# Kernel tuning notes

Hardware: AMD Instinct MI355X
Metric: run time of the kernel (lower is better)

## Reference

```python
import jax, jax.numpy as jnp
import numpy as np
from jax import lax

B, P, DIM, HEADS, K = 2, 4096, 256, 8, 32
DH = DIM // HEADS
SCALE = DH ** -0.5


def setup_inputs() -> dict:
    key = jax.random.key(0)
    ks = jax.random.split(key, 12)
    s = 0.02
    return {
        "xyz": jax.random.uniform(ks[0], (B, P, 3), dtype=jnp.float32),
        "feats": jax.random.normal(ks[1], (B, P, DIM), dtype=jnp.float32),
        "Wq": jax.random.normal(ks[2], (DIM, DIM), dtype=jnp.float32) * s,
        "Wk": jax.random.normal(ks[3], (DIM, DIM), dtype=jnp.float32) * s,
        "Wv": jax.random.normal(ks[4], (DIM, DIM), dtype=jnp.float32) * s,
        "Wp": jax.random.normal(ks[5], (DIM, DIM), dtype=jnp.float32) * s,
        "bp": jnp.zeros((DIM,), jnp.float32),
        "W1": jax.random.normal(ks[6], (DIM, 3), dtype=jnp.float32) * s,
        "b1": jnp.zeros((DIM,), jnp.float32),
        "W2": jax.random.normal(ks[7], (DIM, DIM), dtype=jnp.float32) * s,
        "b2": jnp.zeros((DIM,), jnp.float32),
    }


def _gather(points, idx):
    # points: (B,N,C), idx: (B,M,K) -> (B,M,K,C)
    return jax.vmap(lambda p, i: p[i])(points, idx)


def reference(xyz, feats, Wq, Wk, Wv, Wp, bp, W1, b1, W2, b2):
    b, p, d = feats.shape
    # kNN via squared euclidean distance (same ordering as cdist)
    d2 = jnp.sum((xyz[:, :, None, :] - xyz[:, None, :, :]) ** 2, axis=-1)  # (B,P,P)
    _, idx = lax.top_k(-d2, K)  # (B,P,K) smallest distances

    neigh_xyz = _gather(xyz, idx)                      # (B,P,K,3)
    relpos = neigh_xyz - xyz[:, :, None, :]            # (B,P,K,3)

    q = (feats @ Wq.T).reshape(b, p, HEADS, DH)        # (B,P,H,Dh)
    k_full = feats @ Wk.T                              # (B,P,D)
    v_full = feats @ Wv.T
    k_nei = _gather(k_full, idx).reshape(b, p, K, HEADS, DH)
    v_nei = _gather(v_full, idx).reshape(b, p, K, HEADS, DH)

    # pos MLP: Linear(3,dim) -> ReLU -> Linear(dim,dim)
    h = jax.nn.relu(relpos @ W1.T + b1)
    pos_bias = (h @ W2.T + b2).reshape(b, p, K, HEADS, DH)

    attn = jnp.einsum('bphd,bpkhd->bpkh', q, k_nei + pos_bias) * SCALE
    attn = jax.nn.softmax(attn, axis=2)                # over K neighbors
    out = jnp.einsum('bpkh,bpkhd->bphd', attn, v_nei + pos_bias).reshape(b, p, d)
    return out @ Wp.T + bp
```

## Files before the change

### kernel.cpp

```cpp
#include <hip/hip_runtime.h>
#include <cstddef>

#define PB 4096
static constexpr float SCALE_F = 0.17677669529663687f;

typedef __attribute__((ext_vector_type(8))) short bf16x8;
typedef __attribute__((ext_vector_type(4))) float f32x4;

static __device__ __forceinline__ unsigned short f2bf(float x) {
  unsigned u = __builtin_bit_cast(unsigned, x);
  u += 0x7fffu + ((u >> 16) & 1u);
  return (unsigned short)(u >> 16);
}
static __device__ __forceinline__ float bf2f(unsigned short h) {
  return __builtin_bit_cast(float, (unsigned)h << 16);
}

__global__ __launch_bounds__(64) void knn_kernel(const float* __restrict__ xyz,
                                                 int* __restrict__ idx_out) {
  const int g = blockIdx.x;
  const int b = g >> 12;
  const int p = g & (PB - 1);
  const int lane = threadIdx.x;
  const float* base = xyz + (size_t)b * PB * 3;
  const float qx = base[p * 3 + 0];
  const float qy = base[p * 3 + 1];
  const float qz = base[p * 3 + 2];
  float list_d = 3.4e38f;
  int list_i = -1;
  for (int c = 0; c < PB / 64; ++c) {
    const int j = (c << 6) + lane;
    const float dx = __fsub_rn(qx, base[j * 3 + 0]);
    const float dy = __fsub_rn(qy, base[j * 3 + 1]);
    const float dz = __fsub_rn(qz, base[j * 3 + 2]);
    const float d2 = __fadd_rn(__fadd_rn(__fmul_rn(dx, dx), __fmul_rn(dy, dy)),
                               __fmul_rn(dz, dz));
    float worst = __shfl(list_d, 31);
    unsigned long long mask = __ballot(d2 < worst);
    while (mask) {
      const int l = __ffsll(mask) - 1;
      mask &= mask - 1;
      const float v = __shfl(d2, l);
      worst = __shfl(list_d, 31);
      if (v < worst) {
        const unsigned long long gt = __ballot((lane < 32) && (list_d > v));
        const int pos = __ffsll(gt) - 1;
        const float pd = __shfl_up(list_d, 1);
        const int pi = __shfl_up(list_i, 1);
        if (lane < 32 && lane >= pos) {
          const bool at = (lane == pos);
          list_d = at ? v : pd;
          list_i = at ? ((c << 6) + l) : pi;
        }
      }
    }
  }
  if (lane < 32) idx_out[(size_t)g * 32 + lane] = list_i;
}

__global__ __launch_bounds__(256) void prep_w(
    const float* __restrict__ Wq, const float* __restrict__ Wk,
    const float* __restrict__ Wv, const float* __restrict__ W2,
    const float* __restrict__ Wp,
    unsigned short* __restrict__ whi, unsigned short* __restrict__ wlo) {
  const int e = blockIdx.x * 256 + threadIdx.x;
  const int m = e >> 16;
  const int off = e & 65535;
  const float* src = (m == 0) ? Wq : (m == 1) ? Wk : (m == 2) ? Wv
                     : (m == 3) ? W2 : Wp;
  const float x = src[off];
  const unsigned short hi = f2bf(x);
  whi[e] = hi;
  wlo[e] = f2bf(x - bf2f(hi));
}

static __device__ __forceinline__ void gemm32_mfma(
    const float* __restrict__ A, const unsigned short* __restrict__ wh,
    const unsigned short* __restrict__ wl, const float* __restrict__ bias,
    float* __restrict__ C, const int r0,
    unsigned short* ah, unsigned short* al) {
  const int tid = threadIdx.x;
#pragma unroll
  for (int t = 0; t < 8; ++t) {
    const int idx4 = (t << 8) + tid;
    const int row = idx4 >> 6;
    const int c4 = idx4 & 63;
    const float4 v = *(const float4*)(A + (size_t)(r0 + row) * 256 + (c4 << 2));
    const unsigned short h0 = f2bf(v.x), h1 = f2bf(v.y);
    const unsigned short h2 = f2bf(v.z), h3 = f2bf(v.w);
    const unsigned short l0 = f2bf(v.x - bf2f(h0)), l1 = f2bf(v.y - bf2f(h1));
    const unsigned short l2 = f2bf(v.z - bf2f(h2)), l3 = f2bf(v.w - bf2f(h3));
    const int base = (row << 9) + ((c4 << 3) ^ ((row & 7) << 4));
    *(uint2*)((char*)ah + base) =
        make_uint2((unsigned)h0 | ((unsigned)h1 << 16),
                   (unsigned)h2 | ((unsigned)h3 << 16));
    *(uint2*)((char*)al + base) =
        make_uint2((unsigned)l0 | ((unsigned)l1 << 16),
                   (unsigned)l2 | ((unsigned)l3 << 16));
  }
  __syncthreads();
  const int lane = tid & 63;
  const int w = tid >> 6;
  const int il = lane & 15;
  const int q4 = lane >> 4;
  f32x4 acc[2][4];
#pragma unroll
  for (int mt = 0; mt < 2; ++mt)
#pragma unroll
    for (int nt = 0; nt < 4; ++nt) acc[mt][nt] = (f32x4){0.f, 0.f, 0.f, 0.f};
#pragma unroll 2
  for (int ks = 0; ks < 8; ++ks) {
    bf16x8 bh[4], bl[4], a0[2], a1[2];
#pragma unroll
    for (int nt = 0; nt < 4; ++nt) {
      const int n = (w << 6) + (nt << 4) + il;
      const size_t off = (size_t)n * 256 + (ks << 5) + (q4 << 3);
      bh[nt] = *(const bf16x8*)(wh + off);
      bl[nt] = *(const bf16x8*)(wl + off);
    }
#pragma unroll
    for (int mt = 0; mt < 2; ++mt) {
      const int row = (mt << 4) + il;
      const int byte = (row << 9) + ((((ks << 5) + (q4 << 3)) << 1) ^ ((row & 7) << 4));
      a0[mt] = *(const bf16x8*)((const char*)ah + byte);
      a1[mt] = *(const bf16x8*)((const char*)al + byte);
    }
#pragma unroll
    for (int mt = 0; mt < 2; ++mt)
#pragma unroll
      for (int nt = 0; nt < 4; ++nt) {
        acc[mt][nt] = __builtin_amdgcn_mfma_f32_16x16x32_bf16(a0[mt], bh[nt], acc[mt][nt], 0, 0, 0);
        acc[mt][nt] = __builtin_amdgcn_mfma_f32_16x16x32_bf16(a1[mt], bh[nt], acc[mt][nt], 0, 0, 0);
        acc[mt][nt] = __builtin_amdgcn_mfma_f32_16x16x32_bf16(a0[mt], bl[nt], acc[mt][nt], 0, 0, 0);
      }
  }
#pragma unroll
  for (int mt = 0; mt < 2; ++mt)
#pragma unroll
    for (int nt = 0; nt < 4; ++nt) {
      const int col = (w << 6) + (nt << 4) + il;
      const float bv = bias ? bias[col] : 0.f;
#pragma unroll
      for (int r = 0; r < 4; ++r)
        C[(size_t)(r0 + (mt << 4) + (q4 << 2) + r) * 256 + col] = acc[mt][nt][r] + bv;
    }
}

__global__ __launch_bounds__(256) void qkv_mfma(
    const float* __restrict__ feats,
    const unsigned short* __restrict__ whi, const unsigned short* __restrict__ wlo,
    float* __restrict__ qb, float* __restrict__ kb, float* __restrict__ vb) {
  __shared__ unsigned short ah[32 * 256];
  __shared__ unsigned short al[32 * 256];
  const int bid = blockIdx.x;
  const int sel = bid % 3;
  const int r0 = (bid / 3) << 5;
  const unsigned short* wh = whi + (size_t)sel * 65536;
  const unsigned short* wl = wlo + (size_t)sel * 65536;
  float* C = (sel == 0) ? qb : (sel == 1) ? kb : vb;
  gemm32_mfma(feats, wh, wl, nullptr, C, r0, ah, al);
}

__global__ __launch_bounds__(256) void proj_mfma(
    const float* __restrict__ A,
    const unsigned short* __restrict__ whi, const unsigned short* __restrict__ wlo,
    const float* __restrict__ bp, float* __restrict__ C) {
  __shared__ unsigned short ah[32 * 256];
  __shared__ unsigned short al[32 * 256];
  gemm32_mfma(A, whi, wlo, bp, C, blockIdx.x << 5, ah, al);
}

__global__ __launch_bounds__(512) void fused_kernel(
    const float* __restrict__ xyz, const int* __restrict__ nbr_idx,
    const float* __restrict__ qbuf, const float* __restrict__ kbuf,
    const float* __restrict__ vbuf,
    const float* __restrict__ W1, const float* __restrict__ b1,
    const unsigned short* __restrict__ w2hi, const float* __restrict__ b2,
    float* __restrict__ o_pre) {
  __shared__ unsigned short h_lds[64 * 256];
  __shared__ float q_lds[512];
  __shared__ float rel[2][32][3];
  __shared__ int nbr[2][32];
  __shared__ float sc_lds[2][32][9];
  __shared__ float at_lds[2][32][9];

  const int g0 = blockIdx.x << 1;
  const int b = g0 >> 12;
  const int tid = threadIdx.x;

  if (tid < 64) {
    const int pt = tid >> 5, kk = tid & 31;
    const int gg = g0 + pt;
    const int p = gg & (PB - 1);
    const int j = nbr_idx[(size_t)gg * 32 + kk];
    nbr[pt][kk] = j;
    const float* xb = xyz + (size_t)b * PB * 3;
    rel[pt][kk][0] = xb[j * 3 + 0] - xb[p * 3 + 0];
    rel[pt][kk][1] = xb[j * 3 + 1] - xb[p * 3 + 1];
    rel[pt][kk][2] = xb[j * 3 + 2] - xb[p * 3 + 2];
  }
  q_lds[tid] = qbuf[(size_t)g0 * 256 + tid];
  __syncthreads();

  {
    const int pt = tid >> 8;
    const int half = (tid >> 7) & 1;
    const int cp = tid & 127;
    const int c0 = cp << 1;
    const float w00 = W1[c0 * 3 + 0], w01 = W1[c0 * 3 + 1], w02 = W1[c0 * 3 + 2];
    const float w10 = W1[c0 * 3 + 3], w11 = W1[c0 * 3 + 4], w12 = W1[c0 * 3 + 5];
    const float bb0 = b1[c0], bb1 = b1[c0 + 1];
#pragma unroll 4
    for (int rl = 0; rl < 16; ++rl) {
      const int rloc = (half << 4) + rl;
      const int rr = (pt << 5) + rloc;
      const float rx = rel[pt][rloc][0], ry = rel[pt][rloc][1], rz = rel[pt][rloc][2];
      const float h0 = fmaxf(bb0 + rx * w00 + ry * w01 + rz * w02, 0.f);
      const float h1 = fmaxf(bb1 + rx * w10 + ry * w11 + rz * w12, 0.f);
      const unsigned pk = (unsigned)f2bf(h0) | ((unsigned)f2bf(h1) << 16);
      *(unsigned*)((char*)h_lds + (rr << 9) + (((unsigned)c0 << 1) ^ ((rr & 7) << 4))) = pk;
    }
  }
  __syncthreads();

  const int lane = tid & 63;
  const int w = tid >> 6;
  const int il = lane & 15;
  const int q4 = lane >> 4;

  f32x4 acc[4][2];
#pragma unroll
  for (int mt = 0; mt < 4; ++mt)
#pragma unroll
    for (int nt = 0; nt < 2; ++nt) acc[mt][nt] = (f32x4){0.f, 0.f, 0.f, 0.f};
#pragma unroll 2
  for (int ks = 0; ks < 8; ++ks) {
    bf16x8 bfr[2], afr[4];
#pragma unroll
    for (int nt = 0; nt < 2; ++nt) {
      const int n = (w << 5) + (nt << 4) + il;
      bfr[nt] = *(const bf16x8*)(w2hi + (size_t)n * 256 + (ks << 5) + (q4 << 3));
    }
#pragma unroll
    for (int mt = 0; mt < 4; ++mt) {
      const int row = (mt << 4) + il;
      const int byte = (row << 9) + ((((ks << 5) + (q4 << 3)) << 1) ^ ((row & 7) << 4));
      afr[mt] = *(const bf16x8*)((const char*)h_lds + byte);
    }
#pragma unroll
    for (int mt = 0; mt < 4; ++mt)
#pragma unroll
      for (int nt = 0; nt < 2; ++nt)
        acc[mt][nt] = __builtin_amdgcn_mfma_f32_16x16x32_bf16(
            afr[mt], bfr[nt], acc[mt][nt], 0, 0, 0);
  }
#pragma unroll
  for (int nt = 0; nt < 2; ++nt) {
    const float bv = b2[(w << 5) + (nt << 4) + il];
#pragma unroll
    for (int mt = 0; mt < 4; ++mt)
#pragma unroll
      for (int r = 0; r < 4; ++r) acc[mt][nt][r] += bv;
  }

  const size_t kvbase = (size_t)(b << 12) * 256;

#pragma unroll
  for (int mt = 0; mt < 4; ++mt) {
    const int pt = mt >> 1;
#pragma unroll
    for (int r = 0; r < 4; ++r) {
      const int k = ((mt & 1) << 4) + (q4 << 2) + r;
      const int j = nbr[pt][k];
      const float* krow = kbuf + kvbase + (size_t)j * 256;
      float s = 0.f;
#pragma unroll
      for (int nt = 0; nt < 2; ++nt) {
        const int d = (w << 5) + (nt << 4) + il;
        s += q_lds[(pt << 8) + d] * (krow[d] + acc[mt][nt][r]);
      }
#pragma unroll
      for (int off = 1; off <= 8; off <<= 1) s += __shfl_xor(s, off);
      if (il == 0) sc_lds[pt][k][w] = s * SCALE_F;
    }
  }
  __syncthreads();

  {
    const int kk = tid & 31;
    const int head = (tid >> 5) & 7;
    const int pt = tid >> 8;
    const float val = sc_lds[pt][kk][head];
    float m = val;
#pragma unroll
    for (int off = 16; off; off >>= 1) m = fmaxf(m, __shfl_xor(m, off));
    const float e = __expf(val - m);
    float ssum = e;
#pragma unroll
    for (int off = 16; off; off >>= 1) ssum += __shfl_xor(ssum, off);
    at_lds[pt][kk][head] = e / ssum;
  }
  __syncthreads();

  float o[2][2];
#pragma unroll
  for (int pt = 0; pt < 2; ++pt)
#pragma unroll
    for (int nt = 0; nt < 2; ++nt) o[pt][nt] = 0.f;
#pragma unroll
  for (int mt = 0; mt < 4; ++mt) {
    const int pt = mt >> 1;
#pragma unroll
    for (int r = 0; r < 4; ++r) {
      const int k = ((mt & 1) << 4) + (q4 << 2) + r;
      const int j = nbr[pt][k];
      const float* vrow = vbuf + kvbase + (size_t)j * 256;
      const float aw = at_lds[pt][k][w];
#pragma unroll
      for (int nt = 0; nt < 2; ++nt) {
        const int d = (w << 5) + (nt << 4) + il;
        o[pt][nt] += aw * (vrow[d] + acc[mt][nt][r]);
      }
    }
  }
#pragma unroll
  for (int pt = 0; pt < 2; ++pt)
#pragma unroll
    for (int nt = 0; nt < 2; ++nt) {
      float v = o[pt][nt];
      v += __shfl_xor(v, 16);
      v += __shfl_xor(v, 32);
      if (q4 == 0)
        o_pre[(size_t)(g0 + pt) * 256 + (w << 5) + (nt << 4) + il] = v;
    }
}

extern "C" void kernel_launch(void* const* d_in, const int* in_sizes, int n_in,
                              void* d_out, int out_size, void* d_ws, size_t ws_size,
                              hipStream_t stream) {
  (void)in_sizes; (void)n_in; (void)out_size; (void)ws_size;
  const float* xyz   = (const float*)d_in[0];
  const float* feats = (const float*)d_in[1];
  const float* Wq    = (const float*)d_in[2];
  const float* Wk    = (const float*)d_in[3];
  const float* Wv    = (const float*)d_in[4];
  const float* Wp    = (const float*)d_in[5];
  const float* bp    = (const float*)d_in[6];
  const float* W1    = (const float*)d_in[7];
  const float* b1    = (const float*)d_in[8];
  const float* W2    = (const float*)d_in[9];
  const float* b2    = (const float*)d_in[10];
  float* out = (float*)d_out;

  int* idxw  = (int*)d_ws;
  float* wsf = (float*)d_ws;
  float* qb = wsf + 262144;
  float* kb = qb + 2097152;
  float* vb = kb + 2097152;
  float* op = vb + 2097152;
  unsigned short* whi = (unsigned short*)(op + 2097152);
  unsigned short* wlo = whi + 327680;

  hipLaunchKernelGGL(prep_w, dim3(1280), dim3(256), 0, stream,
                     Wq, Wk, Wv, W2, Wp, whi, wlo);
  hipLaunchKernelGGL(knn_kernel, dim3(2 * PB), dim3(64), 0, stream, xyz, idxw);
  hipLaunchKernelGGL(qkv_mfma, dim3(768), dim3(256), 0, stream,
                     feats, whi, wlo, qb, kb, vb);
  hipLaunchKernelGGL(fused_kernel, dim3(PB), dim3(512), 0, stream,
                     xyz, idxw, qb, kb, vb, W1, b1,
                     whi + (size_t)3 * 65536, b2, op);
  hipLaunchKernelGGL(proj_mfma, dim3(256), dim3(256), 0, stream,
                     op, whi + (size_t)4 * 65536, wlo + (size_t)4 * 65536, bp, out);
}
```

Before: 299.5 us.

## Process one point per block with four waves each covering two heads

The fused attention kernel now handles one query point per 256-thread block instead of two points per 512-thread block, launching twice as many blocks. Each wave computes a 32x64 tile of the positional MLP output (two heads) rather than 64x32, and q values are hoisted into registers. This halves LDS use per block and changes the MFMA tile shape, aiming for better occupancy and fewer A-fragment loads. In exchange, each W2 B-fragment is now reused across only 32 rows, so W2 global/L2 traffic per point roughly doubles.

```diff
diff --git a/kernel.cpp b/kernel.cpp
--- a/kernel.cpp
+++ b/kernel.cpp
@@ -170,51 +170,46 @@
   gemm32_mfma(A, whi, wlo, bp, C, blockIdx.x << 5, ah, al);
 }
 
-__global__ __launch_bounds__(512) void fused_kernel(
+__global__ __launch_bounds__(256) void fused_kernel(
     const float* __restrict__ xyz, const int* __restrict__ nbr_idx,
     const float* __restrict__ qbuf, const float* __restrict__ kbuf,
     const float* __restrict__ vbuf,
     const float* __restrict__ W1, const float* __restrict__ b1,
     const unsigned short* __restrict__ w2hi, const float* __restrict__ b2,
     float* __restrict__ o_pre) {
-  __shared__ unsigned short h_lds[64 * 256];
-  __shared__ float q_lds[512];
-  __shared__ float rel[2][32][3];
-  __shared__ int nbr[2][32];
-  __shared__ float sc_lds[2][32][9];
-  __shared__ float at_lds[2][32][9];
-
-  const int g0 = blockIdx.x << 1;
-  const int b = g0 >> 12;
+  __shared__ unsigned short h_lds[32 * 256];
+  __shared__ float q_lds[256];
+  __shared__ float rel[32][3];
+  __shared__ int nbr[32];
+  __shared__ float sc_lds[32][9];
+  __shared__ float at_lds[32][9];
+
+  const int g = blockIdx.x;
+  const int b = g >> 12;
+  const int p = g & (PB - 1);
   const int tid = threadIdx.x;
 
-  if (tid < 64) {
-    const int pt = tid >> 5, kk = tid & 31;
-    const int gg = g0 + pt;
-    const int p = gg & (PB - 1);
-    const int j = nbr_idx[(size_t)gg * 32 + kk];
-    nbr[pt][kk] = j;
+  if (tid < 32) {
+    const int j = nbr_idx[(size_t)g * 32 + tid];
+    nbr[tid] = j;
     const float* xb = xyz + (size_t)b * PB * 3;
-    rel[pt][kk][0] = xb[j * 3 + 0] - xb[p * 3 + 0];
-    rel[pt][kk][1] = xb[j * 3 + 1] - xb[p * 3 + 1];
-    rel[pt][kk][2] = xb[j * 3 + 2] - xb[p * 3 + 2];
-  }
-  q_lds[tid] = qbuf[(size_t)g0 * 256 + tid];
+    rel[tid][0] = xb[j * 3 + 0] - xb[p * 3 + 0];
+    rel[tid][1] = xb[j * 3 + 1] - xb[p * 3 + 1];
+    rel[tid][2] = xb[j * 3 + 2] - xb[p * 3 + 2];
+  }
+  q_lds[tid] = qbuf[(size_t)g * 256 + tid];
   __syncthreads();
 
   {
-    const int pt = tid >> 8;
-    const int half = (tid >> 7) & 1;
-    const int cp = tid & 127;
-    const int c0 = cp << 1;
+    const int half = tid >> 7;
+    const int c0 = (tid & 127) << 1;
     const float w00 = W1[c0 * 3 + 0], w01 = W1[c0 * 3 + 1], w02 = W1[c0 * 3 + 2];
     const float w10 = W1[c0 * 3 + 3], w11 = W1[c0 * 3 + 4], w12 = W1[c0 * 3 + 5];
     const float bb0 = b1[c0], bb1 = b1[c0 + 1];
 #pragma unroll 4
     for (int rl = 0; rl < 16; ++rl) {
-      const int rloc = (half << 4) + rl;
-      const int rr = (pt << 5) + rloc;
-      const float rx = rel[pt][rloc][0], ry = rel[pt][rloc][1], rz = rel[pt][rloc][2];
+      const int rr = (half << 4) + rl;
+      const float rx = rel[rr][0], ry = rel[rr][1], rz = rel[rr][2];
       const float h0 = fmaxf(bb0 + rx * w00 + ry * w01 + rz * w02, 0.f);
       const float h1 = fmaxf(bb1 + rx * w10 + ry * w11 + rz * w12, 0.f);
       const unsigned pk = (unsigned)f2bf(h0) | ((unsigned)f2bf(h1) << 16);
@@ -228,69 +223,77 @@
   const int il = lane & 15;
   const int q4 = lane >> 4;
 
-  f32x4 acc[4][2];
-#pragma unroll
-  for (int mt = 0; mt < 4; ++mt)
-#pragma unroll
-    for (int nt = 0; nt < 2; ++nt) acc[mt][nt] = (f32x4){0.f, 0.f, 0.f, 0.f};
+  f32x4 acc[2][4];
+#pragma unroll
+  for (int mt = 0; mt < 2; ++mt)
+#pragma unroll
+    for (int nt = 0; nt < 4; ++nt) acc[mt][nt] = (f32x4){0.f, 0.f, 0.f, 0.f};
 #pragma unroll 2
   for (int ks = 0; ks < 8; ++ks) {
-    bf16x8 bfr[2], afr[4];
-#pragma unroll
-    for (int nt = 0; nt < 2; ++nt) {
-      const int n = (w << 5) + (nt << 4) + il;
+    bf16x8 bfr[4], afr[2];
+#pragma unroll
+    for (int nt = 0; nt < 4; ++nt) {
+      const int n = (w << 6) + (nt << 4) + il;
       bfr[nt] = *(const bf16x8*)(w2hi + (size_t)n * 256 + (ks << 5) + (q4 << 3));
     }
 #pragma unroll
-    for (int mt = 0; mt < 4; ++mt) {
+    for (int mt = 0; mt < 2; ++mt) {
       const int row = (mt << 4) + il;
       const int byte = (row << 9) + ((((ks << 5) + (q4 << 3)) << 1) ^ ((row & 7) << 4));
       afr[mt] = *(const bf16x8*)((const char*)h_lds + byte);
     }
 #pragma unroll
-    for (int mt = 0; mt < 4; ++mt)
-#pragma unroll
-      for (int nt = 0; nt < 2; ++nt)
+    for (int mt = 0; mt < 2; ++mt)
+#pragma unroll
+      for (int nt = 0; nt < 4; ++nt)
         acc[mt][nt] = __builtin_amdgcn_mfma_f32_16x16x32_bf16(
             afr[mt], bfr[nt], acc[mt][nt], 0, 0, 0);
   }
 #pragma unroll
-  for (int nt = 0; nt < 2; ++nt) {
-    const float bv = b2[(w << 5) + (nt << 4) + il];
-#pragma unroll
-    for (int mt = 0; mt < 4; ++mt)
+  for (int nt = 0; nt < 4; ++nt) {
+    const float bv = b2[(w << 6) + (nt << 4) + il];
+#pragma unroll
+    for (int mt = 0; mt < 2; ++mt)
 #pragma unroll
       for (int r = 0; r < 4; ++r) acc[mt][nt][r] += bv;
   }
 
   const size_t kvbase = (size_t)(b << 12) * 256;
-
-#pragma unroll
-  for (int mt = 0; mt < 4; ++mt) {
-    const int pt = mt >> 1;
+  float qv[4];
+#pragma unroll
+  for (int nt = 0; nt < 4; ++nt) qv[nt] = q_lds[(w << 6) + (nt << 4) + il];
+
+#pragma unroll
+  for (int mt = 0; mt < 2; ++mt) {
 #pragma unroll
     for (int r = 0; r < 4; ++r) {
-      const int k = ((mt & 1) << 4) + (q4 << 2) + r;
-      const int j = nbr[pt][k];
+      const int k = (mt << 4) + (q4 << 2) + r;
+      const int j = nbr[k];
       const float* krow = kbuf + kvbase + (size_t)j * 256;
-      float s = 0.f;
-#pragma unroll
-      for (int nt = 0; nt < 2; ++nt) {
-        const int d = (w << 5) + (nt << 4) + il;
-        s += q_lds[(pt << 8) + d] * (krow[d] + acc[mt][nt][r]);
-      }
-#pragma unroll
-      for (int off = 1; off <= 8; off <<= 1) s += __shfl_xor(s, off);
-      if (il == 0) sc_lds[pt][k][w] = s * SCALE_F;
+      float sA = 0.f, sB = 0.f;
+#pragma unroll
+      for (int nt = 0; nt < 4; ++nt) {
+        const int d = (w << 6) + (nt << 4) + il;
+        const float t = qv[nt] * (krow[d] + acc[mt][nt][r]);
+        if (nt < 2) sA += t; else sB += t;
+      }
+#pragma unroll
+      for (int off = 1; off <= 8; off <<= 1) {
+        sA += __shfl_xor(sA, off);
+        sB += __shfl_xor(sB, off);
+      }
+      if (il == 0) {
+        sc_lds[k][(w << 1)]     = sA * SCALE_F;
+        sc_lds[k][(w << 1) + 1] = sB * SCALE_F;
+      }
     }
   }
   __syncthreads();
 
   {
     const int kk = tid & 31;
-    const int head = (tid >> 5) & 7;
-    const int pt = tid >> 8;
-    const float val = sc_lds[pt][kk][head];
+    const int head = tid >> 5;
+    const float val = sc_lds[kk][head];
     float m = val;
 #pragma unroll
     for (int off = 16; off; off >>= 1) m = fmaxf(m, __shfl_xor(m, off));
@@ -298,41 +301,38 @@
     float ssum = e;
 #pragma unroll
     for (int off = 16; off; off >>= 1) ssum += __shfl_xor(ssum, off);
-    at_lds[pt][kk][head] = e / ssum;
-  }
-  __syncthreads();
-
-  float o[2][2];
-#pragma unroll
-  for (int pt = 0; pt < 2; ++pt)
-#pragma unroll
-    for (int nt = 0; nt < 2; ++nt) o[pt][nt] = 0.f;
-#pragma unroll
-  for (int mt = 0; mt < 4; ++mt) {
-    const int pt = mt >> 1;
+    at_lds[kk][head] = e / ssum;
+  }
+  __syncthreads();
+
+  float o[4];
+#pragma unroll
+  for (int nt = 0; nt < 4; ++nt) o[nt] = 0.f;
+#pragma unroll
+  for (int mt = 0; mt < 2; ++mt) {
 #pragma unroll
     for (int r = 0; r < 4; ++r) {
-      const int k = ((mt & 1) << 4) + (q4 << 2) + r;
-      const int j = nbr[pt][k];
+      const int k = (mt << 4) + (q4 << 2) + r;
+      const int j = nbr[k];
       const float* vrow = vbuf + kvbase + (size_t)j * 256;
-      const float aw = at_lds[pt][k][w];
-#pragma unroll
-      for (int nt = 0; nt < 2; ++nt) {
-        const int d = (w << 5) + (nt << 4) + il;
-        o[pt][nt] += aw * (vrow[d] + acc[mt][nt][r]);
-      }
-    }
-  }
-#pragma unroll
-  for (int pt = 0; pt < 2; ++pt)
-#pragma unroll
-    for (int nt = 0; nt < 2; ++nt) {
-      float v = o[pt][nt];
-      v += __shfl_xor(v, 16);
-      v += __shfl_xor(v, 32);
-      if (q4 == 0)
-        o_pre[(size_t)(g0 + pt) * 256 + (w << 5) + (nt << 4) + il] = v;
-    }
+      const float awA = at_lds[k][(w << 1)];
+      const float awB = at_lds[k][(w << 1) + 1];
+#pragma unroll
+      for (int nt = 0; nt < 4; ++nt) {
+        const int d = (w << 6) + (nt << 4) + il;
+        const float aw = (nt < 2) ? awA : awB;
+        o[nt] += aw * (vrow[d] + acc[mt][nt][r]);
+      }
+    }
+  }
+#pragma unroll
+  for (int nt = 0; nt < 4; ++nt) {
+    float v = o[nt];
+    v += __shfl_xor(v, 16);
+    v += __shfl_xor(v, 32);
+    if (q4 == 0)
+      o_pre[(size_t)g * 256 + (w << 6) + (nt << 4) + il] = v;
+  }
 }
 
 extern "C" void kernel_launch(void* const* d_in, const int* in_sizes, int n_in,
@@ -366,7 +366,7 @@
   hipLaunchKernelGGL(knn_kernel, dim3(2 * PB), dim3(64), 0, stream, xyz, idxw);
   hipLaunchKernelGGL(qkv_mfma, dim3(768), dim3(256), 0, stream,
                      feats, whi, wlo, qb, kb, vb);
-  hipLaunchKernelGGL(fused_kernel, dim3(PB), dim3(512), 0, stream,
+  hipLaunchKernelGGL(fused_kernel, dim3(2 * PB), dim3(256), 0, stream,
                      xyz, idxw, qb, kb, vb, W1, b1,
                      whi + (size_t)3 * 65536, b2, op);
   hipLaunchKernelGGL(proj_mfma, dim3(256), dim3(256), 0, stream,
```

New measurement: 332.9 us. 1.11x slower.
